# Kernel optimization log

Hardware: AMD Instinct MI355X
Metric: run time of the kernel (lower is better)

Reference implementation:

```python
import jax, jax.numpy as jnp
from jax import lax
import numpy as np

P = 9          # patch_size (hardcoded in CUTSEncoder)
HALF = P // 2  # 4
EPS = 1e-5     # BatchNorm eps (torch default)
SLOPE = 0.01   # LeakyReLU negative slope (torch default)


def _conv(x, w, b):
    # 3x3 'same' conv, NCHW / OIHW
    y = lax.conv_general_dilated(x, w, (1, 1), 'SAME',
                                 dimension_numbers=('NCHW', 'OIHW', 'NCHW'))
    return y + b[None, :, None, None]


def _bn(x, gamma, beta):
    # training-mode BatchNorm2d: batch statistics over (N,H,W)
    m = jnp.mean(x, axis=(0, 2, 3), keepdims=True)
    v = jnp.var(x, axis=(0, 2, 3), keepdims=True)
    return gamma[None, :, None, None] * (x - m) * lax.rsqrt(v + EPS) + beta[None, :, None, None]


def _block(x, w, b, g, be):
    return jax.nn.leaky_relu(_bn(_conv(x, w, b), g, be), SLOPE)


def setup_inputs() -> dict:
    key = jax.random.key(0)
    ks = jax.random.split(key, 16)
    B, C, H, W = 8, 3, 256, 256
    K = 32                 # num_kernels
    L = K * 8              # latent_dim = 256
    S = 32                 # sampled_patches_per_image

    x = jax.random.normal(ks[0], (B, C, H, W), jnp.float32)
    anchors_hw = jax.random.randint(ks[1], (B, S, 2), HALF, H - HALF, jnp.int32)
    positives_hw = jax.random.randint(ks[2], (B, S, 2), HALF, H - HALF, jnp.int32)

    def w_(k, shape):
        return jax.random.normal(k, shape, jnp.float32) * 0.05

    params = {
        'w1': w_(ks[3], (K, C, 3, 3)),       'b1': jnp.zeros((K,), jnp.float32),
        'g1': jnp.ones((K,), jnp.float32),   'be1': jnp.zeros((K,), jnp.float32),
        'w2': w_(ks[4], (2 * K, K, 3, 3)),   'b2': jnp.zeros((2 * K,), jnp.float32),
        'g2': jnp.ones((2 * K,), jnp.float32), 'be2': jnp.zeros((2 * K,), jnp.float32),
        'w3': w_(ks[5], (4 * K, 2 * K, 3, 3)), 'b3': jnp.zeros((4 * K,), jnp.float32),
        'g3': jnp.ones((4 * K,), jnp.float32), 'be3': jnp.zeros((4 * K,), jnp.float32),
        'w4': w_(ks[6], (8 * K, 4 * K, 3, 3)), 'b4': jnp.zeros((8 * K,), jnp.float32),
        'g4': jnp.ones((8 * K,), jnp.float32), 'be4': jnp.zeros((8 * K,), jnp.float32),
        'rw': w_(ks[7], (S * C * P * P, S * L)),  # recon Linear [out,in]
        'rb': jnp.zeros((S * C * P * P,), jnp.float32),
    }
    return dict(x=x, anchors_hw=anchors_hw, positives_hw=positives_hw, **params)


def reference(x, anchors_hw, positives_hw,
              w1, b1, g1, be1, w2, b2, g2, be2,
              w3, b3, g3, be3, w4, b4, g4, be4, rw, rb):
    B, C, H, W = x.shape
    # 4-stage conv+BN+LeakyReLU backbone -> z: [B, L, H, W]
    z = _block(x, w1, b1, g1, be1)
    z = _block(z, w2, b2, g2, be2)
    z = _block(z, w3, b3, g3, be3)
    z = _block(z, w4, b4, g4, be4)

    # batched 9x9 patch extraction around anchors: [B, S, C, P, P]
    def patch(img, hw):  # img: [C,H,W], hw: [2]
        return lax.dynamic_slice(img, (0, hw[0] - HALF, hw[1] - HALF), (C, P, P))
    x_anchors = jax.vmap(lambda img, hws: jax.vmap(lambda hw: patch(img, hw))(hws))(x, anchors_hw)

    # batched pointwise latent gathers: [B, S, L]
    def gather_z(zb, hws):  # zb: [L,H,W]
        return zb[:, hws[:, 0], hws[:, 1]].T  # [S, L]
    z_anchors = jax.vmap(gather_z)(z, anchors_hw)
    z_positives = jax.vmap(gather_z)(z, positives_hw)

    x_anchors_flat = x_anchors.reshape(B, -1)
    x_recon = z_anchors.reshape(B, -1) @ rw.T + rb
    return (z, x_anchors_flat, x_recon, z_anchors, z_positives)
```

## Files before the change

kernel.cpp:

```cpp
#include <hip/hip_runtime.h>
#include <hip/hip_bf16.h>

#define HW 65536
constexpr int IMG_W = 256;

typedef __attribute__((ext_vector_type(8))) short short8;
typedef __attribute__((ext_vector_type(4))) float f32x4;

__device__ __forceinline__ float bf2f(unsigned short u) {
    return __uint_as_float(((unsigned)u) << 16);
}
__device__ __forceinline__ unsigned short f2bf(float f) {
    __hip_bfloat16 h = __float2bfloat16(f);
    return *reinterpret_cast<unsigned short*>(&h);
}

__global__ __launch_bounds__(256) void conv1_direct(
    const float* __restrict__ x, const float* __restrict__ wt,
    const float* __restrict__ bias, unsigned short* __restrict__ outraw)
{
    constexpr int CIN = 3, COUT = 32, OCB = 16;
    const int tile = blockIdx.x;
    const int ty0 = (tile >> 3) << 5;
    const int tx0 = (tile & 7) << 5;
    const int oc0 = blockIdx.y * OCB;
    const int b = blockIdx.z;

    __shared__ alignas(16) float s_in[CIN][34][36];
    __shared__ alignas(16) float s_w[CIN][9][OCB];

    const int tid = threadIdx.x;
    const int lx = tid & 31;
    const int ly = tid >> 5;

    float acc[4][OCB];
    #pragma unroll
    for (int j = 0; j < 4; ++j)
        #pragma unroll
        for (int oc = 0; oc < OCB; ++oc) acc[j][oc] = 0.f;

    for (int idx = tid; idx < CIN * 34 * 34; idx += 256) {
        int ic  = idx / (34 * 34);
        int rem = idx - ic * (34 * 34);
        int r   = rem / 34;
        int cc  = rem - r * 34;
        int gy = ty0 - 1 + r, gx = tx0 - 1 + cc;
        float v = 0.f;
        if ((unsigned)gy < 256u && (unsigned)gx < 256u)
            v = x[((size_t)(b * CIN + ic)) * HW + (size_t)gy * IMG_W + gx];
        s_in[ic][r][cc] = v;
    }
    for (int idx = tid; idx < CIN * 9 * OCB; idx += 256) {
        int oc  = idx & (OCB - 1);
        int t2  = idx >> 4;
        int tap = t2 % 9;
        int ic  = t2 / 9;
        s_w[ic][tap][oc] = wt[((size_t)(oc0 + oc) * CIN + ic) * 9 + tap];
    }
    __syncthreads();

    for (int ic = 0; ic < CIN; ++ic) {
        #pragma unroll
        for (int tap = 0; tap < 9; ++tap) {
            const int dy = tap / 3, dx = tap % 3;
            float wr[OCB];
            #pragma unroll
            for (int q = 0; q < OCB / 4; ++q)
                *(float4*)&wr[q * 4] = *(const float4*)&s_w[ic][tap][q * 4];
            #pragma unroll
            for (int j = 0; j < 4; ++j) {
                float iv = s_in[ic][ly + 8 * j + dy][lx + dx];
                #pragma unroll
                for (int oc = 0; oc < OCB; ++oc) acc[j][oc] += iv * wr[oc];
            }
        }
    }

    #pragma unroll
    for (int j = 0; j < 4; ++j) {
        const size_t p = ((size_t)b << 16) + (size_t)((ty0 + ly + 8 * j) << 8) + tx0 + lx;
        short8 v0, v1;
        #pragma unroll
        for (int k = 0; k < 8; ++k) {
            v0[k] = (short)f2bf(acc[j][k] + bias[oc0 + k]);
            v1[k] = (short)f2bf(acc[j][8 + k] + bias[oc0 + 8 + k]);
        }
        *(short8*)&outraw[p * COUT + oc0]     = v0;
        *(short8*)&outraw[p * COUT + oc0 + 8] = v1;
    }
}

__global__ void repack2(const float* __restrict__ w, unsigned short* __restrict__ wp,
                        int COUT, int CIN)
{
    int i = blockIdx.x * 256 + threadIdx.x;
    int K9 = 9 * CIN;
    if (i >= COUT * K9) return;
    int oc = i / K9, k = i - oc * K9;
    int tap = k / CIN, ic = k - tap * CIN;
    wp[(size_t)(k >> 3) * COUT * 8 + oc * 8 + (k & 7)] =
        f2bf(w[((size_t)(oc * CIN + ic)) * 9 + tap]);
}

template<int CIN, int COUT, int WM, int WN>
__global__ __launch_bounds__(256, 3) void conv_mfma7(
    const unsigned short* __restrict__ in, const float2* __restrict__ coef,
    const unsigned short* __restrict__ wp, const float* __restrict__ bias,
    unsigned short* __restrict__ outraw, float2* __restrict__ partial)
{
    constexpr int WOC = 64;
    constexpr int NG = 4;
    static_assert(WM * WN == 4 && WN * WOC == COUT, "bad wave geometry");
    constexpr int CINP = CIN + 8;
    constexpr int ROWS = WM * 4;
    constexpr int NOCT = CIN / 8;
    constexpr int ICB = CIN / 32;
    constexpr int TILES = 65536 / (ROWS * 16);
    constexpr int NCH = (ROWS + 2) * 18 * NOCT;
    constexpr int CPT = (NCH + 255) / 256;

    __shared__ alignas(16) short s_in[(ROWS + 2) * 18 * CINP];
    __shared__ float2 s_coef[CIN];

    const int tile = blockIdx.x;
    const int b = blockIdx.z;
    const int ty0 = (tile >> 4) * ROWS;
    const int tx0 = (tile & 15) * 16;
    const int tid = threadIdx.x;

    if (tid < CIN) s_coef[tid] = coef[tid];

    const size_t bbase = (size_t)b << 16;
    short8 stg[CPT];
    #pragma unroll
    for (int i = 0; i < CPT; ++i) {
        const int idx = tid + i * 256;
        const int ic8 = idx & (NOCT - 1);
        const int rc  = idx / NOCT;
        const int c = rc % 18, r = rc / 18;
        const int gy = ty0 - 1 + r, gx = tx0 - 1 + c;
        stg[i] = (short8)0;
        if (idx < NCH && (unsigned)gy < 256u && (unsigned)gx < 256u)
            stg[i] = *(const short8*)&in[(bbase + (size_t)(gy << 8) + gx) * CIN + ic8 * 8];
    }
    __syncthreads();

    #pragma unroll
    for (int i = 0; i < CPT; ++i) {
        const int idx = tid + i * 256;
        if (idx < NCH) {
            const int ic8 = idx & (NOCT - 1);
            const int rc  = idx / NOCT;
            const int c = rc % 18, r = rc / 18;
            const int gy = ty0 - 1 + r, gx = tx0 - 1 + c;
            short8 v = (short8)0;
            if ((unsigned)gy < 256u && (unsigned)gx < 256u) {
                #pragma unroll
                for (int j = 0; j < 8; ++j) {
                    float2 ab = s_coef[ic8 * 8 + j];
                    float xv = fmaf(ab.x, bf2f((unsigned short)stg[i][j]), ab.y);
                    xv = fmaxf(xv, 0.01f * xv);
                    v[j] = (short)f2bf(xv);
                }
            }
            *(short8*)&s_in[(r * 18 + c) * CINP + ic8 * 8] = v;
        }
    }
    __syncthreads();

    const int lane = tid & 63;
    const int wv = tid >> 6;
    const int wm = wv / WN, wn = wv % WN;
    const int ln = lane & 15;
    const int grp = lane >> 4;

    f32x4 acc[4][NG] = {};

    const unsigned short* wpb = wp + ((size_t)grp * COUT + wn * WOC + ln) * 8;
    const int fb = (wm * 4) * 18 + ln;

    for (int icb = 0; icb < ICB; ++icb) {
        const int ko = icb * 32 + grp * 8;
        for (int dx = 0; dx < 3; ++dx) {
            short8 frag[6];
            #pragma unroll
            for (int r = 0; r < 6; ++r)
                frag[r] = *(const short8*)&s_in[(fb + r * 18 + dx) * CINP + ko];
            #pragma unroll
            for (int dy = 0; dy < 3; ++dy) {
                const int kc0 = (dy * 3 + dx) * (CIN / 8) + icb * 4;
                short8 wfr[NG];
                #pragma unroll
                for (int g = 0; g < NG; ++g)
                    wfr[g] = *(const short8*)&wpb[((size_t)kc0 * COUT + g * 16) * 8];
                #pragma unroll
                for (int f = 0; f < 4; ++f) {
                    #pragma unroll
                    for (int g = 0; g < NG; ++g)
                        acc[f][g] = __builtin_amdgcn_mfma_f32_16x16x32_bf16(
                            wfr[g], frag[dy + f], acc[f][g], 0, 0, 0);
                }
            }
        }
    }

    const size_t pchunk = ((size_t)(b * TILES + tile) * WM + wm) * COUT;
    #pragma unroll
    for (int g = 0; g < NG; ++g) {
        const int ocl = wn * WOC + g * 16 + grp * 4;
        const f32x4 b4 = *(const f32x4*)&bias[ocl];
        f32x4 vs = {}, vq = {};
        #pragma unroll
        for (int f = 0; f < 4; ++f) {
            const int row = ty0 + wm * 4 + f;
            f32x4 v = acc[f][g] + b4;
            vs += v; vq += v * v;
            short4 sv;
            sv.x = (short)f2bf(v[0]); sv.y = (short)f2bf(v[1]);
            sv.z = (short)f2bf(v[2]); sv.w = (short)f2bf(v[3]);
            *(short4*)&outraw[(bbase + (size_t)(row << 8) + tx0 + ln) * COUT + ocl] = sv;
        }
        #pragma unroll
        for (int d = 1; d < 16; d <<= 1) {
            #pragma unroll
            for (int r = 0; r < 4; ++r) {
                vs[r] += __shfl_xor(vs[r], d);
                vq[r] += __shfl_xor(vq[r], d);
            }
        }
        if (ln == 0) {
            #pragma unroll
            for (int r = 0; r < 4; ++r)
                partial[pchunk + ocl + r] = make_float2(vs[r], vq[r]);
        }
    }
}

template<int C>
__global__ __launch_bounds__(256) void bn_stats_nhwc(const unsigned short* __restrict__ raw,
                                                     float2* __restrict__ partial)
{
    constexpr int CPT = C / 8;
    constexpr int PPI = 256 / CPT;
    const int t = threadIdx.x;
    const int co = t % CPT, pg = t / CPT;
    const int p0 = blockIdx.x * 2048;
    float s[8], ss[8];
    #pragma unroll
    for (int j = 0; j < 8; ++j) { s[j] = 0.f; ss[j] = 0.f; }
    for (int p = p0 + pg; p < p0 + 2048; p += PPI) {
        short8 v = *(const short8*)&raw[(size_t)p * C + co * 8];
        #pragma unroll
        for (int j = 0; j < 8; ++j) {
            float xv = bf2f((unsigned short)v[j]);
            s[j] += xv; ss[j] += xv * xv;
        }
    }
    __shared__ float rs[256][8], rss[256][8];
    #pragma unroll
    for (int j = 0; j < 8; ++j) { rs[t][j] = s[j]; rss[t][j] = ss[j]; }
    __syncthreads();
    for (int off = PPI / 2; off > 0; off >>= 1) {
        if (pg < off) {
            #pragma unroll
            for (int j = 0; j < 8; ++j) {
                rs[t][j]  += rs[t + off * CPT][j];
                rss[t][j] += rss[t + off * CPT][j];
            }
        }
        __syncthreads();
    }
    if (pg == 0) {
        #pragma unroll
        for (int j = 0; j < 8; ++j)
            partial[(size_t)(co * 8 + j) * 256 + blockIdx.x] = make_float2(rs[t][j], rss[t][j]);
    }
}

__global__ void bn_finalize_kernel(const float2* __restrict__ partial,
                                   const float* __restrict__ gamma,
                                   const float* __restrict__ beta,
                                   float2* __restrict__ coef, int C, int nchunk)
{
    int c = threadIdx.x;
    if (c >= C) return;
    float s = 0.f, ss = 0.f;
    for (int i = 0; i < nchunk; ++i) {
        float2 p = partial[(size_t)c * nchunk + i];
        s += p.x; ss += p.y;
    }
    const float N = 524288.f;
    float m = s / N;
    float v = ss / N - m * m;
    float rsq = rsqrtf(v + 1e-5f);
    float a = gamma[c] * rsq;
    coef[c] = make_float2(a, beta[c] - m * a);
}

template<int C, int NCHUNK>
__global__ __launch_bounds__(256) void bn_finalize3(const float2* __restrict__ partial,
                                                    const float* __restrict__ gamma,
                                                    const float* __restrict__ beta,
                                                    float2* __restrict__ coef)
{
    const int c = blockIdx.x, t = threadIdx.x;
    float s = 0.f, q = 0.f;
    for (int i = t; i < NCHUNK; i += 256) {
        float2 p = partial[(size_t)i * C + c];
        s += p.x; q += p.y;
    }
    __shared__ float rs[256], rq[256];
    rs[t] = s; rq[t] = q;
    __syncthreads();
    for (int off = 128; off; off >>= 1) {
        if (t < off) { rs[t] += rs[t + off]; rq[t] += rq[t + off]; }
        __syncthreads();
    }
    if (t == 0) {
        const float N = 524288.f;
        float m = rs[0] / N;
        float v = rq[0] / N - m * m;
        float a = gamma[c] * rsqrtf(v + 1e-5f);
        coef[c] = make_float2(a, beta[c] - m * a);
    }
}

__global__ __launch_bounds__(256) void apply_t(const unsigned short* __restrict__ raw,
                                               const float2* __restrict__ coef,
                                               float* __restrict__ z)
{
    __shared__ float s_t[256 * 36];
    __shared__ float2 s_c[256];
    const int t = threadIdx.x;
    s_c[t] = coef[t];
    __syncthreads();

    const size_t p0 = (size_t)blockIdx.x * 32;
    const int o = t & 31, prow = t >> 5;
    #pragma unroll
    for (int it = 0; it < 4; ++it) {
        const int pxi = prow + it * 8;
        short8 v = *(const short8*)&raw[(p0 + pxi) * 256 + o * 8];
        #pragma unroll
        for (int j = 0; j < 8; ++j) {
            const int oc = o * 8 + j;
            float2 ab = s_c[oc];
            float xv = fmaf(ab.x, bf2f((unsigned short)v[j]), ab.y);
            xv = fmaxf(xv, 0.01f * xv);
            s_t[oc * 36 + (pxi ^ ((o & 7) * 4))] = xv;
        }
    }
    __syncthreads();

    const int Q = t & 7, ocr = t >> 3;
    const int b = (int)(p0 >> 16);
    const int pxl = (int)(p0 & 65535);
    #pragma unroll
    for (int pass = 0; pass < 8; ++pass) {
        const int oc = ocr + pass * 32;
        const int w = (oc >> 3) & 7;
        f32x4 vv = *(const f32x4*)&s_t[oc * 36 + ((Q ^ w) * 4)];
        *(f32x4*)&z[(((size_t)(b * 256 + oc)) << 16) + pxl + Q * 4] = vv;
    }
}

__global__ void patches_kernel(const float* __restrict__ x, const int* __restrict__ hw,
                               float* __restrict__ out)
{
    int bs = blockIdx.x;
    int b = bs >> 5;
    int h = hw[bs * 2], w = hw[bs * 2 + 1];
    int t = threadIdx.x;
    if (t < 243) {
        int c = t / 81, r = (t / 9) % 9, cc = t % 9;
        out[(size_t)bs * 243 + t] =
            x[((size_t)(b * 3 + c)) * HW + (size_t)(h - 4 + r) * IMG_W + (w - 4 + cc)];
    }
}

__global__ void gather_kernel(const float* __restrict__ z, const int* __restrict__ hw,
                              float* __restrict__ out)
{
    int bs = blockIdx.x;
    int b = bs >> 5;
    int h = hw[bs * 2], w = hw[bs * 2 + 1];
    int l = threadIdx.x;
    out[(size_t)bs * 256 + l] = z[((size_t)(b * 256 + l)) * HW + (size_t)h * IMG_W + w];
}

__global__ __launch_bounds__(256) void recon_kernel(const float* __restrict__ za,
                                                    const float* __restrict__ rw,
                                                    const float* __restrict__ rb,
                                                    float* __restrict__ out)
{
    int wave = threadIdx.x >> 6, lane = threadIdx.x & 63;
    int n0 = blockIdx.x * 16 + wave * 4;
    float acc[4][8];
    #pragma unroll
    for (int j = 0; j < 4; ++j)
        #pragma unroll
        for (int bb = 0; bb < 8; ++bb) acc[j][bb] = 0.f;

    for (int i = 0; i < 32; ++i) {
        int k = i * 256 + lane * 4;
        float4 wv[4];
        #pragma unroll
        for (int j = 0; j < 4; ++j)
            wv[j] = *(const float4*)&rw[(size_t)(n0 + j) * 8192 + k];
        #pragma unroll
        for (int bb = 0; bb < 8; ++bb) {
            float4 zv = *(const float4*)&za[(size_t)bb * 8192 + k];
            #pragma unroll
            for (int j = 0; j < 4; ++j)
                acc[j][bb] += zv.x * wv[j].x + zv.y * wv[j].y + zv.z * wv[j].z + zv.w * wv[j].w;
        }
    }
    #pragma unroll
    for (int j = 0; j < 4; ++j)
        #pragma unroll
        for (int bb = 0; bb < 8; ++bb) {
            float v = acc[j][bb];
            #pragma unroll
            for (int off = 32; off; off >>= 1) v += __shfl_down(v, off);
            if (lane == 0) out[(size_t)bb * 7776 + n0 + j] = v + rb[n0 + j];
        }
}

extern "C" void kernel_launch(void* const* d_in, const int* in_sizes, int n_in,
                              void* d_out, int out_size, void* d_ws, size_t ws_size,
                              hipStream_t stream) {
    (void)in_sizes; (void)n_in; (void)out_size; (void)ws_size;

    const float* x        = (const float*)d_in[0];
    const int* anchors    = (const int*)d_in[1];
    const int* positives  = (const int*)d_in[2];
    const float* w1 = (const float*)d_in[3];  const float* b1 = (const float*)d_in[4];
    const float* g1 = (const float*)d_in[5];  const float* be1 = (const float*)d_in[6];
    const float* w2 = (const float*)d_in[7];  const float* b2 = (const float*)d_in[8];
    const float* g2 = (const float*)d_in[9];  const float* be2 = (const float*)d_in[10];
    const float* w3 = (const float*)d_in[11]; const float* b3 = (const float*)d_in[12];
    const float* g3 = (const float*)d_in[13]; const float* be3 = (const float*)d_in[14];
    const float* w4 = (const float*)d_in[15]; const float* b4 = (const float*)d_in[16];
    const float* g4 = (const float*)d_in[17]; const float* be4 = (const float*)d_in[18];
    const float* rw = (const float*)d_in[19]; const float* rb = (const float*)d_in[20];

    float* z  = (float*)d_out;
    float* xa = z + 134217728;
    float* xr = xa + 62208;
    float* za = xr + 62208;
    float* zp = za + 65536;

    char* zb = (char*)d_out;
    unsigned short* raw1 = (unsigned short*)zb;
    unsigned short* raw2 = (unsigned short*)(zb + 33554432ull);
    unsigned short* raw3 = (unsigned short*)(zb + 100663296ull);

    char* ws = (char*)d_ws;
    unsigned short* wp   = (unsigned short*)ws;
    float2* partial = (float2*)(ws + 1048576ull);
    float2* coef1   = (float2*)(ws + 17825792ull);
    float2* coef2   = coef1 + 256;
    float2* coef3   = coef2 + 256;
    float2* coef4   = coef3 + 256;
    unsigned short* raw4 = (unsigned short*)(ws + 18874368ull);

    conv1_direct<<<dim3(64, 2, 8), 256, 0, stream>>>(x, w1, b1, raw1);
    bn_stats_nhwc<32><<<256, 256, 0, stream>>>(raw1, partial);
    bn_finalize_kernel<<<1, 256, 0, stream>>>(partial, g1, be1, coef1, 32, 256);

    repack2<<<(64 * 288 + 255) / 256, 256, 0, stream>>>(w2, wp, 64, 32);
    conv_mfma7<32, 64, 4, 1><<<dim3(256, 1, 8), 256, 0, stream>>>(raw1, coef1, wp, b2, raw2, partial);
    bn_finalize3<64, 8192><<<64, 256, 0, stream>>>(partial, g2, be2, coef2);

    repack2<<<(128 * 576 + 255) / 256, 256, 0, stream>>>(w3, wp, 128, 64);
    conv_mfma7<64, 128, 2, 2><<<dim3(512, 1, 8), 256, 0, stream>>>(raw2, coef2, wp, b3, raw3, partial);
    bn_finalize3<128, 8192><<<128, 256, 0, stream>>>(partial, g3, be3, coef3);

    repack2<<<(256 * 1152 + 255) / 256, 256, 0, stream>>>(w4, wp, 256, 128);
    conv_mfma7<128, 256, 1, 4><<<dim3(1024, 1, 8), 256, 0, stream>>>(raw3, coef3, wp, b4, raw4, partial);
    bn_finalize3<256, 8192><<<256, 256, 0, stream>>>(partial, g4, be4, coef4);

    apply_t<<<16384, 256, 0, stream>>>(raw4, coef4, z);

    patches_kernel<<<256, 256, 0, stream>>>(x, anchors, xa);
    gather_kernel<<<256, 256, 0, stream>>>(z, anchors, za);
    gather_kernel<<<256, 256, 0, stream>>>(z, positives, zp);
    recon_kernel<<<486, 256, 0, stream>>>(za, rw, rb, xr);
}
```

Before: 835.1 us.

## Retile MFMA convs to 16x16 spatial tiles with output-channel blocks and chunked input channels

```diff
diff --git a/kernel.cpp b/kernel.cpp
--- a/kernel.cpp
+++ b/kernel.cpp
@@ -102,112 +102,101 @@
         f2bf(w[((size_t)(oc * CIN + ic)) * 9 + tap]);
 }
 
-template<int CIN, int COUT, int WM, int WN>
-__global__ __launch_bounds__(256, 3) void conv_mfma7(
+template<int CIN, int COUT, int NOC>
+__global__ __launch_bounds__(256, 3) void conv_mfma8(
     const unsigned short* __restrict__ in, const float2* __restrict__ coef,
     const unsigned short* __restrict__ wp, const float* __restrict__ bias,
     unsigned short* __restrict__ outraw, float2* __restrict__ partial)
 {
-    constexpr int WOC = 64;
     constexpr int NG = 4;
-    static_assert(WM * WN == 4 && WN * WOC == COUT, "bad wave geometry");
-    constexpr int CINP = CIN + 8;
-    constexpr int ROWS = WM * 4;
-    constexpr int NOCT = CIN / 8;
-    constexpr int ICB = CIN / 32;
-    constexpr int TILES = 65536 / (ROWS * 16);
-    constexpr int NCH = (ROWS + 2) * 18 * NOCT;
-    constexpr int CPT = (NCH + 255) / 256;
-
-    __shared__ alignas(16) short s_in[(ROWS + 2) * 18 * CINP];
+    constexpr int CH = (CIN < 64) ? CIN : 64;
+    constexpr int KH = CIN / CH;
+    constexpr int CINP = CH + 8;
+    constexpr int NOCT = CH / 8;
+    constexpr int ICB = CH / 32;
+    constexpr int TILES = 256;
+    constexpr int NCH = 18 * 18 * NOCT;
+
+    __shared__ alignas(16) short s_in[18 * 18 * CINP];
     __shared__ float2 s_coef[CIN];
 
-    const int tile = blockIdx.x;
+    const int bx = blockIdx.x;
+    const int tile = bx / NOC;
+    const int oc0 = (bx - tile * NOC) * 64;
     const int b = blockIdx.z;
-    const int ty0 = (tile >> 4) * ROWS;
-    const int tx0 = (tile & 15) * 16;
+    const int ty0 = (tile >> 4) << 4;
+    const int tx0 = (tile & 15) << 4;
     const int tid = threadIdx.x;
 
     if (tid < CIN) s_coef[tid] = coef[tid];
 
+    const int lane = tid & 63;
+    const int wm = tid >> 6;
+    const int ln = lane & 15;
+    const int grp = lane >> 4;
+
+    f32x4 acc[4][NG] = {};
+
     const size_t bbase = (size_t)b << 16;
-    short8 stg[CPT];
-    #pragma unroll
-    for (int i = 0; i < CPT; ++i) {
-        const int idx = tid + i * 256;
-        const int ic8 = idx & (NOCT - 1);
-        const int rc  = idx / NOCT;
-        const int c = rc % 18, r = rc / 18;
-        const int gy = ty0 - 1 + r, gx = tx0 - 1 + c;
-        stg[i] = (short8)0;
-        if (idx < NCH && (unsigned)gy < 256u && (unsigned)gx < 256u)
-            stg[i] = *(const short8*)&in[(bbase + (size_t)(gy << 8) + gx) * CIN + ic8 * 8];
-    }
-    __syncthreads();
-
-    #pragma unroll
-    for (int i = 0; i < CPT; ++i) {
-        const int idx = tid + i * 256;
-        if (idx < NCH) {
+    const unsigned short* wpb = wp + ((size_t)grp * COUT + oc0 + ln) * 8;
+    const int fb = (wm * 4) * 18 + ln;
+
+    for (int kh = 0; kh < KH; ++kh) {
+        __syncthreads();
+
+        for (int idx = tid; idx < NCH; idx += 256) {
             const int ic8 = idx & (NOCT - 1);
             const int rc  = idx / NOCT;
             const int c = rc % 18, r = rc / 18;
             const int gy = ty0 - 1 + r, gx = tx0 - 1 + c;
             short8 v = (short8)0;
             if ((unsigned)gy < 256u && (unsigned)gx < 256u) {
+                short8 rawv = *(const short8*)&in[(bbase + (size_t)(gy << 8) + gx) * CIN
+                                                  + kh * CH + ic8 * 8];
                 #pragma unroll
                 for (int j = 0; j < 8; ++j) {
-                    float2 ab = s_coef[ic8 * 8 + j];
-                    float xv = fmaf(ab.x, bf2f((unsigned short)stg[i][j]), ab.y);
+                    float2 ab = s_coef[kh * CH + ic8 * 8 + j];
+                    float xv = fmaf(ab.x, bf2f((unsigned short)rawv[j]), ab.y);
                     xv = fmaxf(xv, 0.01f * xv);
                     v[j] = (short)f2bf(xv);
                 }
             }
             *(short8*)&s_in[(r * 18 + c) * CINP + ic8 * 8] = v;
         }
-    }
-    __syncthreads();
-
-    const int lane = tid & 63;
-    const int wv = tid >> 6;
-    const int wm = wv / WN, wn = wv % WN;
-    const int ln = lane & 15;
-    const int grp = lane >> 4;
-
-    f32x4 acc[4][NG] = {};
-
-    const unsigned short* wpb = wp + ((size_t)grp * COUT + wn * WOC + ln) * 8;
-    const int fb = (wm * 4) * 18 + ln;
-
-    for (int icb = 0; icb < ICB; ++icb) {
-        const int ko = icb * 32 + grp * 8;
-        for (int dx = 0; dx < 3; ++dx) {
-            short8 frag[6];
-            #pragma unroll
-            for (int r = 0; r < 6; ++r)
-                frag[r] = *(const short8*)&s_in[(fb + r * 18 + dx) * CINP + ko];
-            #pragma unroll
-            for (int dy = 0; dy < 3; ++dy) {
-                const int kc0 = (dy * 3 + dx) * (CIN / 8) + icb * 4;
-                short8 wfr[NG];
+        __syncthreads();
+
+        #pragma unroll
+        for (int icb = 0; icb < ICB; ++icb) {
+            const int ko = icb * 32 + grp * 8;
+            #pragma unroll
+            for (int dx = 0; dx < 3; ++dx) {
+                short8 frag[6];
                 #pragma unroll
-                for (int g = 0; g < NG; ++g)
-                    wfr[g] = *(const short8*)&wpb[((size_t)kc0 * COUT + g * 16) * 8];
+                for (int r = 0; r < 6; ++r)
+                    frag[r] = *(const short8*)&s_in[(fb + r * 18 + dx) * CINP + ko];
                 #pragma unroll
-                for (int f = 0; f < 4; ++f) {
+                for (int dy = 0; dy < 3; ++dy) {
+                    const int kc0 = (dy * 3 + dx) * (CIN / 8) + kh * (CH / 8) + icb * 4;
+                    short8 wfr[NG];
                     #pragma unroll
                     for (int g = 0; g < NG; ++g)
-                        acc[f][g] = __builtin_amdgcn_mfma_f32_16x16x32_bf16(
-                            wfr[g], frag[dy + f], acc[f][g], 0, 0, 0);
+                        wfr[g] = *(const short8*)&wpb[((size_t)kc0 * COUT + g * 16) * 8];
+                    #pragma unroll
+                    for (int f = 0; f < 4; ++f) {
+                        #pragma unroll
+                        for (int g = 0; g < NG; ++g)
+                            acc[f][g] = __builtin_amdgcn_mfma_f32_16x16x32_bf16(
+                                wfr[g], frag[dy + f], acc[f][g], 0, 0, 0);
+                    }
                 }
             }
         }
     }
 
-    const size_t pchunk = ((size_t)(b * TILES + tile) * WM + wm) * COUT;
+    const size_t pchunk = ((size_t)(b * TILES + tile) * 4 + wm) * COUT;
     #pragma unroll
     for (int g = 0; g < NG; ++g) {
-        const int ocl = wn * WOC + g * 16 + grp * 4;
+        const int ocl = oc0 + g * 16 + grp * 4;
         const f32x4 b4 = *(const f32x4*)&bias[ocl];
         f32x4 vs = {}, vq = {};
         #pragma unroll
@@ -469,15 +458,15 @@
     bn_finalize_kernel<<<1, 256, 0, stream>>>(partial, g1, be1, coef1, 32, 256);
 
     repack2<<<(64 * 288 + 255) / 256, 256, 0, stream>>>(w2, wp, 64, 32);
-    conv_mfma7<32, 64, 4, 1><<<dim3(256, 1, 8), 256, 0, stream>>>(raw1, coef1, wp, b2, raw2, partial);
+    conv_mfma8<32, 64, 1><<<dim3(256, 1, 8), 256, 0, stream>>>(raw1, coef1, wp, b2, raw2, partial);
     bn_finalize3<64, 8192><<<64, 256, 0, stream>>>(partial, g2, be2, coef2);
 
     repack2<<<(128 * 576 + 255) / 256, 256, 0, stream>>>(w3, wp, 128, 64);
-    conv_mfma7<64, 128, 2, 2><<<dim3(512, 1, 8), 256, 0, stream>>>(raw2, coef2, wp, b3, raw3, partial);
+    conv_mfma8<64, 128, 2><<<dim3(512, 1, 8), 256, 0, stream>>>(raw2, coef2, wp, b3, raw3, partial);
     bn_finalize3<128, 8192><<<128, 256, 0, stream>>>(partial, g3, be3, coef3);
 
     repack2<<<(256 * 1152 + 255) / 256, 256, 0, stream>>>(w4, wp, 256, 128);
-    conv_mfma7<128, 256, 1, 4><<<dim3(1024, 1, 8), 256, 0, stream>>>(raw3, coef3, wp, b4, raw4, partial);
+    conv_mfma8<128, 256, 4><<<dim3(1024, 1, 8), 256, 0, stream>>>(raw3, coef3, wp, b4, raw4, partial);
     bn_finalize3<256, 8192><<<256, 256, 0, stream>>>(partial, g4, be4, coef4);
 
     apply_t<<<16384, 256, 0, stream>>>(raw4, coef4, z);
```

Measured after the change: 934.7 us. +11.9%, slower.
